# Kernel optimization log

Hardware: AMD Instinct MI355X
Metric: run time of the kernel (lower is better)

## Reference

```python
import jax, jax.numpy as jnp
import numpy as np

NUM_HEADS = 8

def _ln(x):
    m = x.mean(-1, keepdims=True)
    v = ((x - m) ** 2).mean(-1, keepdims=True)
    return (x - m) / jnp.sqrt(v + 1e-5)

def _encoder_layer(x, qkv_w, out_w, w1, w2, attn_mask=None):
    # standard post-LN transformer encoder layer; returns output and
    # head-averaged attention probabilities (b, t, t)
    b, t, d = x.shape
    dh = d // NUM_HEADS
    qkv = jnp.einsum('btd,cde->cbte', x, qkv_w)          # (3, b, t, d)
    q, k, v = [a.reshape(b, t, NUM_HEADS, dh).transpose(0, 2, 1, 3) for a in qkv]
    scores = jnp.einsum('bhqd,bhkd->bhqk', q, k) / jnp.sqrt(jnp.asarray(dh, x.dtype))
    if attn_mask is not None:
        scores = scores + attn_mask                       # additive -inf/0 mask
    probs = jax.nn.softmax(scores, axis=-1)
    ctx = jnp.einsum('bhqk,bhkd->bhqd', probs, v)
    ctx = ctx.transpose(0, 2, 1, 3).reshape(b, t, d)
    x = _ln(x + ctx @ out_w)
    x = _ln(x + jax.nn.relu(x @ w1) @ w2)
    return x, probs.mean(axis=1)

def _window_ids(wbool):
    # faithful vectorization of generate_local_window_mask_v2's sequential scan:
    # run-length segmentation of the thresholded weights, where a run of
    # length 1 is absorbed into the following run (weights[frame_start] is
    # overwritten). Returns per-frame window id (T,) int32.
    T = wbool.shape[0]
    def step(carry, t):
        cur, start, wid = carry
        wt = wbool[t]
        same = wt == cur
        merge = (~same) & (start + 1 == t)   # length-1 run absorbed
        close = (~same) & (~merge)           # close window, start new one
        cur = jnp.where(same, cur, wt)
        start = jnp.where(close, t, start)
        wid = wid + close.astype(jnp.int32)
        return (cur, start, wid), wid
    _, ids = jax.lax.scan(step, (wbool[0], jnp.int32(0), jnp.int32(0)), jnp.arange(1, T))
    return jnp.concatenate([jnp.zeros((1,), jnp.int32), ids])

def reference(x, v_qkv_w, v_out_w, v_w1, v_w2, l_qkv_w, l_out_w, l_w1, l_w2):
    b, t, d = x.shape
    # 1) vanilla transformer pass
    out_v, aw_v = _encoder_layer(x, v_qkv_w, v_out_w, v_w1, v_w2)
    # attention received per key token, min-max normalized (normalize_tensor)
    w = aw_v.sum(axis=1)                                   # (b, t)
    wmin = w.min(axis=-1, keepdims=True)
    wmax = w.max(axis=-1, keepdims=True)
    w = (w - wmin) / (wmax - wmin + 1e-8)
    # 2) dynamic window mask generation (threshold = 0.5)
    ids = jax.vmap(_window_ids)(w >= 0.5)                  # (b, t)
    same = ids[:, :, None] == ids[:, None, :]
    attn_mask = jnp.where(same, 0.0, -jnp.inf).astype(x.dtype)   # (b, t, t)
    # window_mapping[b, k, j] = 1 if frame j belongs to window k
    # (kept at full t rows; torch truncates to max_window_count, which is
    #  data-dependent; extra rows here are all-zero)
    window_mapping = (jnp.arange(t, dtype=jnp.int32)[None, :, None] == ids[:, None, :]).astype(x.dtype)
    # 3) dynamic-local-window transformer pass with block-diagonal mask
    out_l, aw_l = _encoder_layer(out_v, l_qkv_w, l_out_w, l_w1, l_w2,
                                 attn_mask=attn_mask[:, None])  # broadcast over heads
    aw_l = jnp.where(jnp.isneginf(aw_l), jnp.zeros_like(aw_l), aw_l)
    wl = jax.nn.softmax(aw_l.sum(axis=1), axis=-1)         # (b, t)
    # 4) window-weighted pooling
    word_tokens = jnp.einsum('bwt,btd->bwd', window_mapping, out_l * wl[:, :, None])
    return jnp.concatenate([word_tokens, x], axis=1), window_mapping

def setup_inputs() -> dict:
    B, T, D, FF = 8, 1024, 512, 2048
    key = jax.random.key(0)
    ks = jax.random.split(key, 9)
    s = 0.02
    return {
        'x': jax.random.normal(ks[0], (B, T, D), jnp.float32),
        'v_qkv_w': jax.random.normal(ks[1], (3, D, D), jnp.float32) * s,
        'v_out_w': jax.random.normal(ks[2], (D, D), jnp.float32) * s,
        'v_w1': jax.random.normal(ks[3], (D, FF), jnp.float32) * s,
        'v_w2': jax.random.normal(ks[4], (FF, D), jnp.float32) * s,
        'l_qkv_w': jax.random.normal(ks[5], (3, D, D), jnp.float32) * s,
        'l_out_w': jax.random.normal(ks[6], (D, D), jnp.float32) * s,
        'l_w1': jax.random.normal(ks[7], (D, FF), jnp.float32) * s,
        'l_w2': jax.random.normal(ks[8], (FF, D), jnp.float32) * s,
    }
```

## Files before the change

kernel.cpp:

```cpp
#include <hip/hip_runtime.h>
#include <math.h>

#define Bz 8
#define Tz 1024
#define Dz 512
#define FFz 2048
#define Hz 8
#define DHz 64
#define Mz (Bz * Tz)

typedef __attribute__((ext_vector_type(8))) short short8;
typedef __attribute__((ext_vector_type(4))) float f32x4;

__device__ inline unsigned short f2bf(float f) {
  unsigned u = __builtin_bit_cast(unsigned, f);
  return (unsigned short)((u + 0x7FFFu + ((u >> 16) & 1u)) >> 16);
}
__device__ inline float bf2f(unsigned short h) {
  unsigned u = (unsigned)h << 16;
  return __builtin_bit_cast(float, u);
}

__device__ inline void gll16(const unsigned short* g, unsigned short* l) {
  __builtin_amdgcn_global_load_lds(
      (const __attribute__((address_space(1))) void*)g,
      (__attribute__((address_space(3))) void*)l, 16, 0, 0);
}

__device__ inline void attn_decode(int g, int& b, int& h, int& qt) {
  const int xcd = g & 7;
  const int j = g >> 3;
  qt = j & 15;
  const int bh = ((j >> 4) << 3) | xcd;
  b = bh >> 3;
  h = bh & 7;
}

__device__ inline int swz(int row, int slotByte) {
  return row * 128 + (slotByte ^ ((row & 7) << 4));
}

struct WDesc { const float* src; unsigned short* dst; unsigned short* dstlo;
               int K; int N; int blk0; };
struct PrepArgs { WDesc d[12]; int nwc; };

__global__ __launch_bounds__(256) void prep_kernel(PrepArgs P,
    const float* __restrict__ x, unsigned short* __restrict__ xbf,
    unsigned short* __restrict__ xlo, float* __restrict__ csz)
{
  const int bid = blockIdx.x;
  const int tid = threadIdx.x;
  if (bid < P.nwc) {
    int i = 0;
    while (i < 11 && bid >= P.d[i + 1].blk0) ++i;
    const WDesc w = P.d[i];
    const int lb = bid - w.blk0;
    const int nbn = w.N / 32;
    const int bn = (lb % nbn) * 32, bk = (lb / nbn) * 32;
    __shared__ float t[32][33];
    const int tx = tid & 31, ty = tid >> 5;
#pragma unroll
    for (int r = 0; r < 32; r += 8)
      t[ty + r][tx] = w.src[(size_t)(bk + ty + r) * w.N + bn + tx];
    __syncthreads();
#pragma unroll
    for (int r = 0; r < 32; r += 8) {
      float v = t[tx][ty + r];
      unsigned short hv = f2bf(v);
      w.dst[(size_t)(bn + ty + r) * w.K + bk + tx] = hv;
      if (w.dstlo)
        w.dstlo[(size_t)(bn + ty + r) * w.K + bk + tx] = f2bf(v - bf2f(hv));
    }
  } else if (bid < P.nwc + 64) {
    int idx = (bid - P.nwc) * 256 + tid;
    csz[idx] = 0.f;
  } else {
    int i = (bid - P.nwc - 64) * 256 + tid;
    float4 v = *reinterpret_cast<const float4*>(&x[(size_t)i * 4]);
    ushort4 o, ol;
    o.x = f2bf(v.x); o.y = f2bf(v.y); o.z = f2bf(v.z); o.w = f2bf(v.w);
    ol.x = f2bf(v.x - bf2f(o.x)); ol.y = f2bf(v.y - bf2f(o.y));
    ol.z = f2bf(v.z - bf2f(o.z)); ol.w = f2bf(v.w - bf2f(o.w));
    *reinterpret_cast<ushort4*>(&xbf[(size_t)i * 4]) = o;
    *reinterpret_cast<ushort4*>(&xlo[(size_t)i * 4]) = ol;
  }
}

__global__ __launch_bounds__(256) void mfma_gemm_kernel(
    const unsigned short* __restrict__ A, const unsigned short* __restrict__ BT,
    void* __restrict__ p1, void* __restrict__ p2, void* __restrict__ p3,
    int K, int N, int mode)
{
  __shared__ unsigned short As[128 * 32];
  __shared__ unsigned short Bs[128 * 32];
  const int tid = threadIdx.x;
  const int lane = tid & 63, wave = tid >> 6;
  const int mr = lane & 15, quad = lane >> 4;
  const int wr = wave >> 1, wc = wave & 1;
  const int m0 = blockIdx.y * 128;
  const int n0 = blockIdx.x * 128;

  f32x4 acc[4][4];
  const f32x4 zero = {0.f, 0.f, 0.f, 0.f};
#pragma unroll
  for (int i = 0; i < 4; ++i)
#pragma unroll
    for (int j = 0; j < 4; ++j) acc[i][j] = zero;

  const int lrow = lane >> 2, lslot = lane & 3;
  const unsigned short* Ag0 = A + (size_t)(m0 + wave * 16 + lrow) * K + lslot * 8;
  const unsigned short* Ag1 = A + (size_t)(m0 + 64 + wave * 16 + lrow) * K + lslot * 8;
  const unsigned short* Bg0 = BT + (size_t)(n0 + wave * 16 + lrow) * K + lslot * 8;
  const unsigned short* Bg1 = BT + (size_t)(n0 + 64 + wave * 16 + lrow) * K + lslot * 8;
  unsigned short* Al0 = As + wave * 512;
  unsigned short* Al1 = As + 2048 + wave * 512;
  unsigned short* Bl0 = Bs + wave * 512;
  unsigned short* Bl1 = Bs + 2048 + wave * 512;
  char* AsB = (char*)As;
  char* BsB = (char*)Bs;

  for (int k0 = 0; k0 < K; k0 += 32) {
    gll16(Ag0 + k0, Al0);
    gll16(Ag1 + k0, Al1);
    gll16(Bg0 + k0, Bl0);
    gll16(Bg1 + k0, Bl1);
    __syncthreads();
    short8 af[4], bf[4];
#pragma unroll
    for (int i = 0; i < 4; ++i)
      af[i] = *reinterpret_cast<const short8*>(AsB + (wr * 64 + i * 16 + mr) * 64 + quad * 16);
#pragma unroll
    for (int j = 0; j < 4; ++j)
      bf[j] = *reinterpret_cast<const short8*>(BsB + (wc * 64 + j * 16 + mr) * 64 + quad * 16);
#pragma unroll
    for (int i = 0; i < 4; ++i)
#pragma unroll
      for (int j = 0; j < 4; ++j)
        acc[i][j] = __builtin_amdgcn_mfma_f32_16x16x32_bf16(af[i], bf[j], acc[i][j], 0, 0, 0);
    __syncthreads();
  }

  const int m0w = m0 + wr * 64;
  const int n0w = n0 + wc * 64;
  int emode = mode;
  unsigned short* Cbf = (unsigned short*)p1;
  unsigned short* Vt  = (unsigned short*)p1;
  int ncol = N, coff = 0;
  if (mode == 5) {
    if (n0w < 512)       { emode = 1; Cbf = (unsigned short*)p1; ncol = 512; coff = 0; }
    else if (n0w < 1024) { emode = 1; Cbf = (unsigned short*)p2; ncol = 512; coff = 512; }
    else                 { emode = 4; Vt = (unsigned short*)p3; coff = 1024; }
  }
  if (emode == 4) {
#pragma unroll
    for (int i = 0; i < 4; ++i)
#pragma unroll
      for (int j = 0; j < 4; ++j) {
        const int col = n0w - coff + j * 16 + mr;
        const int row0 = m0w + i * 16 + quad * 4;
        const int bb = row0 >> 10, t0 = row0 & 1023;
        ushort4 pk;
        pk.x = f2bf(acc[i][j][0]); pk.y = f2bf(acc[i][j][1]);
        pk.z = f2bf(acc[i][j][2]); pk.w = f2bf(acc[i][j][3]);
        *reinterpret_cast<ushort4*>(
            &Vt[((size_t)((bb * Hz + (col >> 6)) * DHz + (col & 63))) * Tz + t0]) = pk;
      }
  } else if (emode == 0) {
    float* Cf = (float*)p1;
#pragma unroll
    for (int i = 0; i < 4; ++i)
#pragma unroll
      for (int j = 0; j < 4; ++j) {
        const int col = n0w + j * 16 + mr;
#pragma unroll
        for (int rr = 0; rr < 4; ++rr)
          Cf[(size_t)(m0w + i * 16 + quad * 4 + rr) * N + col] = acc[i][j][rr];
      }
  } else {
    const bool relu = (emode == 2);
#pragma unroll
    for (int i = 0; i < 4; ++i)
#pragma unroll
      for (int j = 0; j < 4; ++j) {
        const int col = n0w - coff + j * 16 + mr;
#pragma unroll
        for (int rr = 0; rr < 4; ++rr) {
          float v = acc[i][j][rr];
          if (relu) v = fmaxf(v, 0.f);
          Cbf[(size_t)(m0w + i * 16 + quad * 4 + rr) * ncol + col] = f2bf(v);
        }
      }
  }
}

__global__ __launch_bounds__(256) void gemm_qk_mfma_kernel(
    const unsigned short* __restrict__ Xh, const unsigned short* __restrict__ Xl,
    const unsigned short* __restrict__ WQh, const unsigned short* __restrict__ WQl,
    const unsigned short* __restrict__ WKh, const unsigned short* __restrict__ WKl,
    unsigned short* __restrict__ Qhi, unsigned short* __restrict__ Qlo,
    unsigned short* __restrict__ Khi, unsigned short* __restrict__ Klo)
{
  __shared__ unsigned short Ash[128 * 32];
  __shared__ unsigned short Asl[128 * 32];
  __shared__ unsigned short Bsh[128 * 32];
  __shared__ unsigned short Bsl[128 * 32];
  const int tid = threadIdx.x;
  const int lane = tid & 63, wave = tid >> 6;
  const int mr = lane & 15, quad = lane >> 4;
  const int wr = wave >> 1, wc = wave & 1;
  const int sel = blockIdx.y >> 6;
  const int m0 = (blockIdx.y & 63) * 128;
  const int n0 = blockIdx.x * 128;
  const unsigned short* Bh = sel ? WKh : WQh;
  const unsigned short* Bl = sel ? WKl : WQl;
  unsigned short* Chi = sel ? Khi : Qhi;
  unsigned short* Clo = sel ? Klo : Qlo;

  f32x4 acc[4][4];
  const f32x4 zero = {0.f, 0.f, 0.f, 0.f};
#pragma unroll
  for (int i = 0; i < 4; ++i)
#pragma unroll
    for (int j = 0; j < 4; ++j) acc[i][j] = zero;

  const int lrow = lane >> 2, lslot = lane & 3;
  const unsigned short* gAh0 = Xh + (size_t)(m0 + wave * 16 + lrow) * Dz + lslot * 8;
  const unsigned short* gAh1 = Xh + (size_t)(m0 + 64 + wave * 16 + lrow) * Dz + lslot * 8;
  const unsigned short* gAl0 = Xl + (size_t)(m0 + wave * 16 + lrow) * Dz + lslot * 8;
  const unsigned short* gAl1 = Xl + (size_t)(m0 + 64 + wave * 16 + lrow) * Dz + lslot * 8;
  const unsigned short* gBh0 = Bh + (size_t)(n0 + wave * 16 + lrow) * Dz + lslot * 8;
  const unsigned short* gBh1 = Bh + (size_t)(n0 + 64 + wave * 16 + lrow) * Dz + lslot * 8;
  const unsigned short* gBl0 = Bl + (size_t)(n0 + wave * 16 + lrow) * Dz + lslot * 8;
  const unsigned short* gBl1 = Bl + (size_t)(n0 + 64 + wave * 16 + lrow) * Dz + lslot * 8;
  unsigned short* LAh0 = Ash + wave * 512; unsigned short* LAh1 = Ash + 2048 + wave * 512;
  unsigned short* LAl0 = Asl + wave * 512; unsigned short* LAl1 = Asl + 2048 + wave * 512;
  unsigned short* LBh0 = Bsh + wave * 512; unsigned short* LBh1 = Bsh + 2048 + wave * 512;
  unsigned short* LBl0 = Bsl + wave * 512; unsigned short* LBl1 = Bsl + 2048 + wave * 512;
  char* AhB = (char*)Ash; char* AlB = (char*)Asl;
  char* BhB = (char*)Bsh; char* BlB = (char*)Bsl;

  for (int k0 = 0; k0 < Dz; k0 += 32) {
    gll16(gAh0 + k0, LAh0); gll16(gAh1 + k0, LAh1);
    gll16(gAl0 + k0, LAl0); gll16(gAl1 + k0, LAl1);
    gll16(gBh0 + k0, LBh0); gll16(gBh1 + k0, LBh1);
    gll16(gBl0 + k0, LBl0); gll16(gBl1 + k0, LBl1);
    __syncthreads();
    short8 ah[4], al[4], bh[4], bl[4];
#pragma unroll
    for (int i = 0; i < 4; ++i) {
      const int ab = (wr * 64 + i * 16 + mr) * 64 + quad * 16;
      ah[i] = *reinterpret_cast<const short8*>(AhB + ab);
      al[i] = *reinterpret_cast<const short8*>(AlB + ab);
    }
#pragma unroll
    for (int j = 0; j < 4; ++j) {
      const int bb = (wc * 64 + j * 16 + mr) * 64 + quad * 16;
      bh[j] = *reinterpret_cast<const short8*>(BhB + bb);
      bl[j] = *reinterpret_cast<const short8*>(BlB + bb);
    }
#pragma unroll
    for (int i = 0; i < 4; ++i)
#pragma unroll
      for (int j = 0; j < 4; ++j) {
        acc[i][j] = __builtin_amdgcn_mfma_f32_16x16x32_bf16(al[i], bh[j], acc[i][j], 0, 0, 0);
        acc[i][j] = __builtin_amdgcn_mfma_f32_16x16x32_bf16(ah[i], bl[j], acc[i][j], 0, 0, 0);
        acc[i][j] = __builtin_amdgcn_mfma_f32_16x16x32_bf16(ah[i], bh[j], acc[i][j], 0, 0, 0);
      }
    __syncthreads();
  }

  const int m0w = m0 + wr * 64;
  const int n0w = n0 + wc * 64;
#pragma unroll
  for (int i = 0; i < 4; ++i)
#pragma unroll
    for (int j = 0; j < 4; ++j) {
      const int col = n0w + j * 16 + mr;
#pragma unroll
      for (int rr = 0; rr < 4; ++rr) {
        const size_t row = (size_t)(m0w + i * 16 + quad * 4 + rr);
        float v = acc[i][j][rr];
        unsigned short hv = f2bf(v);
        Chi[row * Dz + col] = hv;
        Clo[row * Dz + col] = f2bf(v - bf2f(hv));
      }
    }
}

__global__ __launch_bounds__(256) void attn_z_kernel(
    const unsigned short* __restrict__ Qh, const unsigned short* __restrict__ Kh,
    float* __restrict__ invzG)
{
  __shared__ unsigned short Ksh[64 * 64];
  const int tid = threadIdx.x;
  const int lane = tid & 63, wave = tid >> 6;
  const int c = lane & 15, quad = lane >> 4;
  int b, h, qt;
  attn_decode(blockIdx.x, b, h, qt);
  const size_t bT = (size_t)b * Tz;
  const int qrow = qt * 64 + wave * 16;
  const int hoff = h * DHz;

  const size_t qbase = (bT + qrow + c) * Dz + hoff + quad * 8;
  short8 q0 = *reinterpret_cast<const short8*>(Qh + qbase);
  short8 q1 = *reinterpret_cast<const short8*>(Qh + qbase + 32);

  const int sr = tid >> 3;
  const int sj = (tid & 7) * 16;
  const unsigned short* khb = Kh + (bT + sr) * Dz + hoff + (tid & 7) * 8;
  char* KshB = (char*)Ksh;

  const f32x4 zf = {0.f, 0.f, 0.f, 0.f};
  float z[4] = {0.f, 0.f, 0.f, 0.f};

  for (int t = 0; t < 16; ++t) {
    const int k0 = t * 64;
    short8 g0 = *reinterpret_cast<const short8*>(khb + (size_t)k0 * Dz);
    short8 g1 = *reinterpret_cast<const short8*>(khb + (size_t)(k0 + 32) * Dz);
    *reinterpret_cast<short8*>(KshB + swz(sr, sj)) = g0;
    *reinterpret_cast<short8*>(KshB + swz(sr + 32, sj)) = g1;
    __syncthreads();
#pragma unroll
    for (int sub = 0; sub < 4; ++sub) {
      const int row = sub * 16 + c;
      short8 kh0 = *reinterpret_cast<const short8*>(KshB + swz(row, quad * 16));
      short8 kh1 = *reinterpret_cast<const short8*>(KshB + swz(row, 64 + quad * 16));
      f32x4 aA = zf, aB = zf;
      aA = __builtin_amdgcn_mfma_f32_16x16x32_bf16(q0, kh0, aA, 0, 0, 0);
      aB = __builtin_amdgcn_mfma_f32_16x16x32_bf16(q1, kh1, aB, 0, 0, 0);
#pragma unroll
      for (int rr = 0; rr < 4; ++rr) z[rr] += __expf((aA[rr] + aB[rr]) * 0.125f);
    }
    __syncthreads();
  }
#pragma unroll
  for (int w = 1; w < 16; w <<= 1) {
#pragma unroll
    for (int rr = 0; rr < 4; ++rr) z[rr] += __shfl_xor(z[rr], w);
  }
  if (c == 0) {
#pragma unroll
    for (int rr = 0; rr < 4; ++rr)
      invzG[(size_t)(b * Hz + h) * Tz + qrow + quad * 4 + rr] = 1.f / z[rr];
  }
}

__global__ __launch_bounds__(256) void attn_ctx_kernel(
    const unsigned short* __restrict__ Qh, const unsigned short* __restrict__ Ql,
    const unsigned short* __restrict__ Kh, const unsigned short* __restrict__ Kl,
    const unsigned short* __restrict__ Vt, const float* __restrict__ invzG,
    unsigned short* __restrict__ ctx, float* __restrict__ part)
{
  __shared__ unsigned short Ksh[64 * 64];
  __shared__ unsigned short Ksl[64 * 64];
  __shared__ unsigned short Vsh[64 * 64];
  __shared__ unsigned short Pld[64][76];
  __shared__ float CSPt[4][64];
  const int tid = threadIdx.x;
  const int lane = tid & 63, wave = tid >> 6;
  const int c = lane & 15, quad = lane >> 4;
  int b, h, qt;
  attn_decode(blockIdx.x, b, h, qt);
  const size_t bT = (size_t)b * Tz;
  const int qrow = qt * 64 + wave * 16;
  const int hoff = h * DHz;
  const int lidx = b * 128 + h * 16 + qt;

  const size_t qbase = (bT + qrow + c) * Dz + hoff + quad * 8;
  short8 q0h = *reinterpret_cast<const short8*>(Qh + qbase);
  short8 q1h = *reinterpret_cast<const short8*>(Qh + qbase + 32);
  short8 q0l = *reinterpret_cast<const short8*>(Ql + qbase);
  short8 q1l = *reinterpret_cast<const short8*>(Ql + qbase + 32);

  float invz[4];
#pragma unroll
  for (int rr = 0; rr < 4; ++rr)
    invz[rr] = invzG[(size_t)(b * Hz + h) * Tz + qrow + quad * 4 + rr];

  const int sr = tid >> 3;
  const int sj = (tid & 7) * 16;
  const unsigned short* khb = Kh + (bT + sr) * Dz + hoff + (tid & 7) * 8;
  const unsigned short* klb = Kl + (bT + sr) * Dz + hoff + (tid & 7) * 8;
  const unsigned short* vtb = Vt + ((size_t)(b * Hz + h) * DHz + sr) * Tz + (tid & 7) * 8;

  const f32x4 zf = {0.f, 0.f, 0.f, 0.f};
  f32x4 ot[4] = {zf, zf, zf, zf};

  char* KshB = (char*)Ksh;
  char* KslB = (char*)Ksl;
  char* VshB = (char*)Vsh;

  for (int t = 0; t < 16; ++t) {
    const int k0 = t * 64;
    short8 g0 = *reinterpret_cast<const short8*>(khb + (size_t)k0 * Dz);
    short8 g1 = *reinterpret_cast<const short8*>(khb + (size_t)(k0 + 32) * Dz);
    short8 g2 = *reinterpret_cast<const short8*>(klb + (size_t)k0 * Dz);
    short8 g3 = *reinterpret_cast<const short8*>(klb + (size_t)(k0 + 32) * Dz);
    short8 g4 = *reinterpret_cast<const short8*>(vtb + k0);
    short8 g5 = *reinterpret_cast<const short8*>(vtb + 32 * Tz + k0);
    *reinterpret_cast<short8*>(KshB + swz(sr, sj)) = g0;
    *reinterpret_cast<short8*>(KshB + swz(sr + 32, sj)) = g1;
    *reinterpret_cast<short8*>(KslB + swz(sr, sj)) = g2;
    *reinterpret_cast<short8*>(KslB + swz(sr + 32, sj)) = g3;
    *reinterpret_cast<short8*>(VshB + swz(sr, sj)) = g4;
    *reinterpret_cast<short8*>(VshB + swz(sr + 32, sj)) = g5;
    __syncthreads();

#pragma unroll
    for (int sub = 0; sub < 4; ++sub) {
      const int row = sub * 16 + c;
      short8 kh0 = *reinterpret_cast<const short8*>(KshB + swz(row, quad * 16));
      short8 kh1 = *reinterpret_cast<const short8*>(KshB + swz(row, 64 + quad * 16));
      short8 kl0 = *reinterpret_cast<const short8*>(KslB + swz(row, quad * 16));
      short8 kl1 = *reinterpret_cast<const short8*>(KslB + swz(row, 64 + quad * 16));
      f32x4 aA = zf, aB = zf;
      aA = __builtin_amdgcn_mfma_f32_16x16x32_bf16(q0h, kh0, aA, 0, 0, 0);
      aB = __builtin_amdgcn_mfma_f32_16x16x32_bf16(q1h, kh1, aB, 0, 0, 0);
      aA = __builtin_amdgcn_mfma_f32_16x16x32_bf16(q0h, kl0, aA, 0, 0, 0);
      aB = __builtin_amdgcn_mfma_f32_16x16x32_bf16(q1h, kl1, aB, 0, 0, 0);
      aA = __builtin_amdgcn_mfma_f32_16x16x32_bf16(q0l, kh0, aA, 0, 0, 0);
      aB = __builtin_amdgcn_mfma_f32_16x16x32_bf16(q1l, kh1, aB, 0, 0, 0);
      float p[4];
#pragma unroll
      for (int rr = 0; rr < 4; ++rr)
        p[rr] = __expf((aA[rr] + aB[rr]) * 0.125f) * invz[rr];
      float cs = p[0] + p[1] + p[2] + p[3];
      cs += __shfl_xor(cs, 16);
      cs += __shfl_xor(cs, 32);
      if (quad == 0) CSPt[wave][sub * 16 + c] = cs;
#pragma unroll
      for (int rr = 0; rr < 4; ++rr)
        Pld[(wave << 4) + quad * 4 + rr][sub * 16 + c] = f2bf(p[rr]);
    }

    union { short8 v; ushort4 hh[2]; } pb0, pb1;
    pb0.hh[0] = *reinterpret_cast<const ushort4*>(&Pld[(wave << 4) + c][quad * 8]);
    pb0.hh[1] = *reinterpret_cast<const ushort4*>(&Pld[(wave << 4) + c][quad * 8 + 4]);
    pb1.hh[0] = *reinterpret_cast<const ushort4*>(&Pld[(wave << 4) + c][32 + quad * 8]);
    pb1.hh[1] = *reinterpret_cast<const ushort4*>(&Pld[(wave << 4) + c][32 + quad * 8 + 4]);
#pragma unroll
    for (int ds = 0; ds < 4; ++ds) {
      const int row = ds * 16 + c;
      short8 v0 = *reinterpret_cast<const short8*>(VshB + swz(row, quad * 16));
      short8 v1 = *reinterpret_cast<const short8*>(VshB + swz(row, 64 + quad * 16));
      ot[ds] = __builtin_amdgcn_mfma_f32_16x16x32_bf16(v0, pb0.v, ot[ds], 0, 0, 0);
      ot[ds] = __builtin_amdgcn_mfma_f32_16x16x32_bf16(v1, pb1.v, ot[ds], 0, 0, 0);
    }
    __syncthreads();

    if (tid < 64) {
      float v = ((CSPt[0][tid] + CSPt[1][tid]) + CSPt[2][tid]) + CSPt[3][tid];
      part[(size_t)lidx * 1024 + k0 + tid] = v * (1.f / Hz);
    }
  }

  const size_t cb = (bT + qrow + c) * Dz + hoff;
#pragma unroll
  for (int ds = 0; ds < 4; ++ds) {
    ushort4 pk;
    pk.x = f2bf(ot[ds][0]); pk.y = f2bf(ot[ds][1]);
    pk.z = f2bf(ot[ds][2]); pk.w = f2bf(ot[ds][3]);
    *reinterpret_cast<ushort4*>(&ctx[cb + ds * 16 + quad * 4]) = pk;
  }
}

__global__ __launch_bounds__(256) void colsum_reduce_kernel(
    const float* __restrict__ part, float* __restrict__ colsum)
{
  const int i = blockIdx.x * 256 + threadIdx.x;
  const int b = i >> 10, k = i & 1023;
  const float* p = part + (size_t)(b * 128) * 1024 + k;
  float s = 0.f;
  for (int j = 0; j < 128; ++j) s += p[(size_t)j * 1024];
  colsum[i] = s;
}

__global__ __launch_bounds__(256) void attn_mfma2_kernel(
    const unsigned short* __restrict__ Qh, const unsigned short* __restrict__ Kh,
    const unsigned short* __restrict__ Vt, const int* __restrict__ ids,
    const int* __restrict__ wst,
    unsigned short* __restrict__ ctx, float* __restrict__ colsum)
{
  __shared__ unsigned short Ksh[64 * 64];
  __shared__ unsigned short Vsh[64 * 64];
  __shared__ unsigned short Pld[64][76];
  __shared__ float csb[1024];

  const int tid = threadIdx.x;
  const int lane = tid & 63, wave = tid >> 6;
  const int c = lane & 15, quad = lane >> 4;
  int b, h, qt;
  attn_decode(blockIdx.x, b, h, qt);
  const size_t bT = (size_t)b * Tz;
  const int qrow = qt * 64 + wave * 16;
  const int hoff = h * DHz;

  for (int i = tid; i < 1024; i += 256) csb[i] = 0.f;

  const int id_lo = ids[bT + qt * 64];
  const int id_hi = ids[bT + qt * 64 + 63];
  const int klo = wst[b * (Tz + 1) + id_lo];
  const int khi = wst[b * (Tz + 1) + id_hi + 1];
  const int t0 = klo >> 6, t1 = (khi - 1) >> 6;

  const size_t qbase = (bT + qrow + c) * Dz + hoff + quad * 8;
  short8 q0 = *reinterpret_cast<const short8*>(Qh + qbase);
  short8 q1 = *reinterpret_cast<const short8*>(Qh + qbase + 32);

  int qid[4];
#pragma unroll
  for (int rr = 0; rr < 4; ++rr) qid[rr] = ids[bT + qrow + quad * 4 + rr];

  const int sr = tid >> 3;
  const int sj = (tid & 7) * 16;
  const unsigned short* khb = Kh + (bT + sr) * Dz + hoff + (tid & 7) * 8;
  const unsigned short* vtb = Vt + ((size_t)(b * Hz + h) * DHz + sr) * Tz + (tid & 7) * 8;
  char* KshB = (char*)Ksh;
  char* VshB = (char*)Vsh;
  __syncthreads();

  const f32x4 zf = {0.f, 0.f, 0.f, 0.f};

  float z[4] = {0.f, 0.f, 0.f, 0.f};
  for (int t = t0; t <= t1; ++t) {
    const int k0 = t * 64;
    short8 g0 = *reinterpret_cast<const short8*>(khb + (size_t)k0 * Dz);
    short8 g1 = *reinterpret_cast<const short8*>(khb + (size_t)(k0 + 32) * Dz);
    *reinterpret_cast<short8*>(KshB + swz(sr, sj)) = g0;
    *reinterpret_cast<short8*>(KshB + swz(sr + 32, sj)) = g1;
    __syncthreads();
#pragma unroll
    for (int sub = 0; sub < 4; ++sub) {
      const int row = sub * 16 + c;
      short8 kh0 = *reinterpret_cast<const short8*>(KshB + swz(row, quad * 16));
      short8 kh1 = *reinterpret_cast<const short8*>(KshB + swz(row, 64 + quad * 16));
      f32x4 acc = zf;
      acc = __builtin_amdgcn_mfma_f32_16x16x32_bf16(q0, kh0, acc, 0, 0, 0);
      acc = __builtin_amdgcn_mfma_f32_16x16x32_bf16(q1, kh1, acc, 0, 0, 0);
      int kidv = ids[bT + k0 + sub * 16 + c];
#pragma unroll
      for (int rr = 0; rr < 4; ++rr) {
        float e = __expf(acc[rr] * 0.125f);
        if (qid[rr] != kidv) e = 0.f;
        z[rr] += e;
      }
    }
    __syncthreads();
  }
#pragma unroll
  for (int w = 1; w < 16; w <<= 1) {
#pragma unroll
    for (int rr = 0; rr < 4; ++rr) z[rr] += __shfl_xor(z[rr], w);
  }
  float invz[4];
#pragma unroll
  for (int rr = 0; rr < 4; ++rr) invz[rr] = 1.f / z[rr];

  f32x4 ot[4] = {zf, zf, zf, zf};
  for (int t = t0; t <= t1; ++t) {
    const int k0 = t * 64;
    short8 g0 = *reinterpret_cast<const short8*>(khb + (size_t)k0 * Dz);
    short8 g1 = *reinterpret_cast<const short8*>(khb + (size_t)(k0 + 32) * Dz);
    short8 g4 = *reinterpret_cast<const short8*>(vtb + k0);
    short8 g5 = *reinterpret_cast<const short8*>(vtb + 32 * Tz + k0);
    *reinterpret_cast<short8*>(KshB + swz(sr, sj)) = g0;
    *reinterpret_cast<short8*>(KshB + swz(sr + 32, sj)) = g1;
    *reinterpret_cast<short8*>(VshB + swz(sr, sj)) = g4;
    *reinterpret_cast<short8*>(VshB + swz(sr + 32, sj)) = g5;
    __syncthreads();
#pragma unroll
    for (int sub = 0; sub < 4; ++sub) {
      const int row = sub * 16 + c;
      short8 kh0 = *reinterpret_cast<const short8*>(KshB + swz(row, quad * 16));
      short8 kh1 = *reinterpret_cast<const short8*>(KshB + swz(row, 64 + quad * 16));
      f32x4 acc = zf;
      acc = __builtin_amdgcn_mfma_f32_16x16x32_bf16(q0, kh0, acc, 0, 0, 0);
      acc = __builtin_amdgcn_mfma_f32_16x16x32_bf16(q1, kh1, acc, 0, 0, 0);
      int kidv = ids[bT + k0 + sub * 16 + c];
      float p[4];
#pragma unroll
      for (int rr = 0; rr < 4; ++rr) {
        float e = __expf(acc[rr] * 0.125f);
        if (qid[rr] != kidv) e = 0.f;
        p[rr] = e * invz[rr];
      }
      float cs = p[0] + p[1] + p[2] + p[3];
      cs += __shfl_xor(cs, 16);
      cs += __shfl_xor(cs, 32);
      if (quad == 0) atomicAdd(&csb[k0 + sub * 16 + c], cs);
#pragma unroll
      for (int rr = 0; rr < 4; ++rr)
        Pld[(wave << 4) + quad * 4 + rr][sub * 16 + c] = f2bf(p[rr]);
    }
    union { short8 v; ushort4 hh[2]; } pb0, pb1;
    pb0.hh[0] = *reinterpret_cast<const ushort4*>(&Pld[(wave << 4) + c][quad * 8]);
    pb0.hh[1] = *reinterpret_cast<const ushort4*>(&Pld[(wave << 4) + c][quad * 8 + 4]);
    pb1.hh[0] = *reinterpret_cast<const ushort4*>(&Pld[(wave << 4) + c][32 + quad * 8]);
    pb1.hh[1] = *reinterpret_cast<const ushort4*>(&Pld[(wave << 4) + c][32 + quad * 8 + 4]);
#pragma unroll
    for (int ds = 0; ds < 4; ++ds) {
      const int row = ds * 16 + c;
      short8 v0 = *reinterpret_cast<const short8*>(VshB + swz(row, quad * 16));
      short8 v1 = *reinterpret_cast<const short8*>(VshB + swz(row, 64 + quad * 16));
      ot[ds] = __builtin_amdgcn_mfma_f32_16x16x32_bf16(v0, pb0.v, ot[ds], 0, 0, 0);
      ot[ds] = __builtin_amdgcn_mfma_f32_16x16x32_bf16(v1, pb1.v, ot[ds], 0, 0, 0);
    }
    __syncthreads();
  }

  const size_t cb = (bT + qrow + c) * Dz + hoff;
#pragma unroll
  for (int ds = 0; ds < 4; ++ds) {
    ushort4 pk;
    pk.x = f2bf(ot[ds][0]); pk.y = f2bf(ot[ds][1]);
    pk.z = f2bf(ot[ds][2]); pk.w = f2bf(ot[ds][3]);
    *reinterpret_cast<ushort4*>(&ctx[cb + ds * 16 + quad * 4]) = pk;
  }
  __syncthreads();
  for (int i = tid; i < 1024; i += 256)
    atomicAdd(&colsum[bT + i], csb[i] * (1.f / Hz));
}

__global__ __launch_bounds__(256) void ln_kernel(const float* __restrict__ residf,
    const unsigned short* __restrict__ residbf, const float* __restrict__ delta,
    float* __restrict__ outf, unsigned short* __restrict__ outbf)
{
  const size_t base = (size_t)blockIdx.x * Dz;
  const int tid = threadIdx.x;
  float r0, r1;
  if (residf) {
    r0 = residf[base + tid]; r1 = residf[base + tid + 256];
  } else {
    r0 = bf2f(residbf[base + tid]); r1 = bf2f(residbf[base + tid + 256]);
  }
  float x0 = r0 + delta[base + tid];
  float x1 = r1 + delta[base + tid + 256];
  __shared__ float red[4];
  float s = x0 + x1;
#pragma unroll
  for (int off = 32; off; off >>= 1) s += __shfl_down(s, off);
  if ((tid & 63) == 0) red[tid >> 6] = s;
  __syncthreads();
  const float mean = (red[0] + red[1] + red[2] + red[3]) * (1.f / Dz);
  __syncthreads();
  float d0 = x0 - mean, d1 = x1 - mean;
  float v = d0 * d0 + d1 * d1;
#pragma unroll
  for (int off = 32; off; off >>= 1) v += __shfl_down(v, off);
  if ((tid & 63) == 0) red[tid >> 6] = v;
  __syncthreads();
  const float var = (red[0] + red[1] + red[2] + red[3]) * (1.f / Dz);
// ... 118 lines not shown
    const int b = bid >> 10;
    float a0 = 0.f, a1 = 0.f;
    if (w < nwin[b]) {
      const int s = wst[b * (Tz + 1) + w], e = wst[b * (Tz + 1) + w + 1];
      for (int t = s; t < e; ++t) {
        const float sc = wl[b * Tz + t];
        const unsigned short* p = &outl[((size_t)(b * Tz + t)) * Dz];
        a0 += bf2f(p[tid]) * sc;
        a1 += bf2f(p[tid + 256]) * sc;
      }
    }
    float* o = &out[((size_t)(b * 2 * Tz + w)) * Dz];
    o[tid] = a0;
    o[tid + 256] = a1;
  } else if (bid < 16384) {
    const int lb = bid - 8192;
    const int w = lb & (Tz - 1);
    const int b = lb >> 10;
    const int j = tid * 4;
    int4 id4 = *reinterpret_cast<const int4*>(&ids[b * Tz + j]);
    float4 v;
    v.x = (id4.x == w) ? 1.f : 0.f;
    v.y = (id4.y == w) ? 1.f : 0.f;
    v.z = (id4.z == w) ? 1.f : 0.f;
    v.w = (id4.w == w) ? 1.f : 0.f;
    *reinterpret_cast<float4*>(&out2[((size_t)(b * Tz + w)) * Tz + j]) = v;
  } else {
    size_t i = (size_t)(bid - 16384) * 256 + tid;
    size_t idx = i * 4;
    size_t rowi = idx >> 9;
    size_t d = idx & 511;
    size_t b = rowi >> 10, t = rowi & 1023;
    float4 v = *reinterpret_cast<const float4*>(&x[idx]);
    *reinterpret_cast<float4*>(&out[(((b * 2 * Tz) + Tz + t) << 9) + d]) = v;
  }
}

extern "C" void kernel_launch(void* const* d_in, const int* in_sizes, int n_in,
                              void* d_out, int out_size, void* d_ws, size_t ws_size,
                              hipStream_t stream)
{
  (void)in_sizes; (void)n_in; (void)out_size; (void)ws_size;
  const float* x     = (const float*)d_in[0];
  const float* vqkv  = (const float*)d_in[1];
  const float* voutw = (const float*)d_in[2];
  const float* vw1   = (const float*)d_in[3];
  const float* vw2   = (const float*)d_in[4];
  const float* lqkv  = (const float*)d_in[5];
  const float* loutw = (const float*)d_in[6];
  const float* lw1   = (const float*)d_in[7];
  const float* lw2   = (const float*)d_in[8];
  float* out = (float*)d_out;
  float* ws  = (float*)d_ws;

  unsigned short* QLbf = (unsigned short*)(ws + 0);
  unsigned short* KLbf = (unsigned short*)(ws + 2097152);
  float* PROJ = ws + 0;
  float* Y1   = ws + 4194304;
  unsigned short* QHbf = (unsigned short*)(ws + 8388608);
  unsigned short* KHbf = (unsigned short*)(ws + 10485760);
  unsigned short* VT   = (unsigned short*)(ws + 12582912);
  unsigned short* SLOT1 = (unsigned short*)(ws + 14680064);
  unsigned short* SLOT2 = (unsigned short*)(ws + 16777216);
  unsigned short* HIDbf = (unsigned short*)(ws + 18874368);
  unsigned short* XBF   = (unsigned short*)(ws + 18874368);
  float* PART = ws + 18874368;
  unsigned short* XLO = (unsigned short*)(ws + 20971520);
  unsigned short* WVQV = (unsigned short*)(ws + 27262976);
  unsigned short* WVO  = (unsigned short*)(ws + 27394048);
  unsigned short* WV1  = (unsigned short*)(ws + 27525120);
  unsigned short* WV2  = (unsigned short*)(ws + 28049408);
  unsigned short* WLQ0 = (unsigned short*)(ws + 28573696);
  unsigned short* WLQ1 = (unsigned short*)(ws + 28704768);
  unsigned short* WLQ2 = (unsigned short*)(ws + 28835840);
  unsigned short* WLO  = (unsigned short*)(ws + 28966912);
  unsigned short* WL1  = (unsigned short*)(ws + 29097984);
  unsigned short* WL2  = (unsigned short*)(ws + 29622272);
  float* CS1   = ws + 30146560;
  float* CS2   = ws + 30154752;
  float* WLs   = ws + 30162944;
  int*   IDS   = (int*)(ws + 30171136);
  int*   WST   = (int*)(ws + 30179328);
  int*   NWIN  = (int*)(ws + 30187776);
  float* INVZ  = ws + 30195968;
  unsigned short* WQH = (unsigned short*)(ws + 30261504);
  unsigned short* WQL = (unsigned short*)(ws + 30392576);
  unsigned short* WKH = (unsigned short*)(ws + 30523648);
  unsigned short* WKL = (unsigned short*)(ws + 30654720);

  dim3 blk(256);

  PrepArgs P;
  auto setw = [&](int i, const float* s, unsigned short* d, unsigned short* dl,
                  int K, int N, int b0) {
    P.d[i].src = s; P.d[i].dst = d; P.d[i].dstlo = dl;
    P.d[i].K = K; P.d[i].N = N; P.d[i].blk0 = b0;
  };
  int b0 = 0;
  setw(0, vqkv + 2 * Dz * Dz, WVQV, nullptr, Dz, Dz, b0); b0 += 256;
  setw(1, voutw, WVO, nullptr, Dz, Dz, b0); b0 += 256;
  setw(2, vw1, WV1, nullptr, Dz, FFz, b0); b0 += 1024;
  setw(3, vw2, WV2, nullptr, FFz, Dz, b0); b0 += 1024;
  setw(4, lqkv + 0 * Dz * Dz, WLQ0, nullptr, Dz, Dz, b0); b0 += 256;
  setw(5, lqkv + 1 * Dz * Dz, WLQ1, nullptr, Dz, Dz, b0); b0 += 256;
  setw(6, lqkv + 2 * Dz * Dz, WLQ2, nullptr, Dz, Dz, b0); b0 += 256;
  setw(7, loutw, WLO, nullptr, Dz, Dz, b0); b0 += 256;
  setw(8, lw1, WL1, nullptr, Dz, FFz, b0); b0 += 1024;
  setw(9, lw2, WL2, nullptr, FFz, Dz, b0); b0 += 1024;
  setw(10, vqkv + 0 * Dz * Dz, WQH, WQL, Dz, Dz, b0); b0 += 256;
  setw(11, vqkv + 1 * Dz * Dz, WKH, WKL, Dz, Dz, b0); b0 += 256;
  P.nwc = b0;
  prep_kernel<<<dim3(P.nwc + 64 + 4096), blk, 0, stream>>>(P, x, XBF, XLO, CS1);

  auto mgemm = [&](const unsigned short* A, const unsigned short* BT, void* p1,
                   void* p2, void* p3, int K, int N, int mode) {
    mfma_gemm_kernel<<<dim3(N / 128, Mz / 128), dim3(256), 0, stream>>>(
        A, BT, p1, p2, p3, K, N, mode);
  };

  gemm_qk_mfma_kernel<<<dim3(4, 128), dim3(256), 0, stream>>>(
      XBF, XLO, WQH, WQL, WKH, WKL, QHbf, QLbf, KHbf, KLbf);
  attn_z_kernel<<<dim3(Bz * Hz * 16), blk, 0, stream>>>(QHbf, KHbf, INVZ);
  mgemm(XBF, WVQV, VT, nullptr, nullptr, Dz, Dz, 4);
  attn_ctx_kernel<<<dim3(Bz * Hz * 16), blk, 0, stream>>>(
      QHbf, QLbf, KHbf, KLbf, VT, INVZ, SLOT1, PART);
  colsum_reduce_kernel<<<dim3(32), blk, 0, stream>>>(PART, CS1);
  window_ids_kernel<<<dim3(Bz), blk, 0, stream>>>(CS1, IDS, WST, NWIN);
  mgemm(SLOT1, WVO, PROJ, nullptr, nullptr, Dz, Dz, 0);
  ln_kernel<<<dim3(Mz), blk, 0, stream>>>(x, nullptr, PROJ, Y1, SLOT2);
  mgemm(SLOT2, WV1, HIDbf, nullptr, nullptr, Dz, FFz, 2);
  mgemm(HIDbf, WV2, PROJ, nullptr, nullptr, FFz, Dz, 0);
  ln_kernel<<<dim3(Mz), blk, 0, stream>>>(Y1, nullptr, PROJ, nullptr, SLOT2);

  mgemm(SLOT2, WLQ0, QHbf, KHbf, VT, Dz, 3 * Dz, 5);
  attn_mfma2_kernel<<<dim3(Bz * Hz * 16), blk, 0, stream>>>(
      QHbf, KHbf, VT, IDS, WST, SLOT1, CS2);
  mgemm(SLOT1, WLO, PROJ, nullptr, nullptr, Dz, Dz, 0);
  ln_kernel<<<dim3(Mz), blk, 0, stream>>>(nullptr, SLOT2, PROJ, Y1, SLOT2);
  mgemm(SLOT2, WL1, HIDbf, nullptr, nullptr, Dz, FFz, 2);
  mgemm(HIDbf, WL2, PROJ, nullptr, nullptr, FFz, Dz, 0);
  ln_kernel<<<dim3(Mz), blk, 0, stream>>>(Y1, nullptr, PROJ, nullptr, SLOT2);

  wl_softmax_kernel<<<dim3(Bz), blk, 0, stream>>>(CS2, WLs);
  outputs_kernel<<<dim3(20480), blk, 0, stream>>>(SLOT2, WLs, WST, NWIN, IDS, x,
                                                  out, out + (size_t)Bz * 2 * Tz * Dz);
}
```

Measured before the change: 582.5 us.

## Widen GEMM K-tile to 64 with swizzled LDS, fuse attention normalizer pass, use async LDS loads

The GEMM kernels now stage a 64-wide K slice per iteration into an XOR-swizzled LDS layout, which halves the number of barriers and should reduce bank conflicts. LDS use per block doubles. The separate attention normalizer kernel is folded into the context kernel as a first pass, removing one launch and the INVZ round-trip through memory. The attention kernels also switch from register-staged global loads to direct global-to-LDS loads with a matching swizzle.

```diff
diff --git a/kernel.cpp b/kernel.cpp
--- a/kernel.cpp
+++ b/kernel.cpp
@@ -91,8 +91,8 @@
     void* __restrict__ p1, void* __restrict__ p2, void* __restrict__ p3,
     int K, int N, int mode)
 {
-  __shared__ unsigned short As[128 * 32];
-  __shared__ unsigned short Bs[128 * 32];
+  __shared__ unsigned short As[128 * 64];
+  __shared__ unsigned short Bs[128 * 64];
   const int tid = threadIdx.x;
   const int lane = tid & 63, wave = tid >> 6;
   const int mr = lane & 15, quad = lane >> 4;
@@ -107,36 +107,42 @@
 #pragma unroll
     for (int j = 0; j < 4; ++j) acc[i][j] = zero;
 
-  const int lrow = lane >> 2, lslot = lane & 3;
-  const unsigned short* Ag0 = A + (size_t)(m0 + wave * 16 + lrow) * K + lslot * 8;
-  const unsigned short* Ag1 = A + (size_t)(m0 + 64 + wave * 16 + lrow) * K + lslot * 8;
-  const unsigned short* Bg0 = BT + (size_t)(n0 + wave * 16 + lrow) * K + lslot * 8;
-  const unsigned short* Bg1 = BT + (size_t)(n0 + 64 + wave * 16 + lrow) * K + lslot * 8;
-  unsigned short* Al0 = As + wave * 512;
-  unsigned short* Al1 = As + 2048 + wave * 512;
-  unsigned short* Bl0 = Bs + wave * 512;
-  unsigned short* Bl1 = Bs + 2048 + wave * 512;
+  const int r8 = lane >> 3;
+  const int s8 = (lane & 7) ^ r8;
+  const unsigned short* Agb = A + (size_t)(m0 + wave * 8 + r8) * K + s8 * 8;
+  const unsigned short* Bgb = BT + (size_t)(n0 + wave * 8 + r8) * K + s8 * 8;
+  unsigned short* Adb = As + wave * 512;
+  unsigned short* Bdb = Bs + wave * 512;
   char* AsB = (char*)As;
   char* BsB = (char*)Bs;
-
-  for (int k0 = 0; k0 < K; k0 += 32) {
-    gll16(Ag0 + k0, Al0);
-    gll16(Ag1 + k0, Al1);
-    gll16(Bg0 + k0, Bl0);
-    gll16(Bg1 + k0, Bl1);
-    __syncthreads();
-    short8 af[4], bf[4];
-#pragma unroll
-    for (int i = 0; i < 4; ++i)
-      af[i] = *reinterpret_cast<const short8*>(AsB + (wr * 64 + i * 16 + mr) * 64 + quad * 16);
-#pragma unroll
-    for (int j = 0; j < 4; ++j)
-      bf[j] = *reinterpret_cast<const short8*>(BsB + (wc * 64 + j * 16 + mr) * 64 + quad * 16);
-#pragma unroll
-    for (int i = 0; i < 4; ++i)
+  const int xr = (mr & 7) << 4;
+
+  for (int k0 = 0; k0 < K; k0 += 64) {
+#pragma unroll
+    for (int p = 0; p < 4; ++p) {
+      gll16(Agb + (size_t)(p * 32) * K + k0, Adb + p * 2048);
+      gll16(Bgb + (size_t)(p * 32) * K + k0, Bdb + p * 2048);
+    }
+    __syncthreads();
+    short8 af[2][4], bf[2][4];
+#pragma unroll
+    for (int hh = 0; hh < 2; ++hh) {
+#pragma unroll
+      for (int i = 0; i < 4; ++i)
+        af[hh][i] = *reinterpret_cast<const short8*>(
+            AsB + (wr * 64 + i * 16 + mr) * 128 + ((((hh << 2) + quad) << 4) ^ xr));
 #pragma unroll
       for (int j = 0; j < 4; ++j)
-        acc[i][j] = __builtin_amdgcn_mfma_f32_16x16x32_bf16(af[i], bf[j], acc[i][j], 0, 0, 0);
+        bf[hh][j] = *reinterpret_cast<const short8*>(
+            BsB + (wc * 64 + j * 16 + mr) * 128 + ((((hh << 2) + quad) << 4) ^ xr));
+    }
+#pragma unroll
+    for (int hh = 0; hh < 2; ++hh)
+#pragma unroll
+      for (int i = 0; i < 4; ++i)
+#pragma unroll
+        for (int j = 0; j < 4; ++j)
+          acc[i][j] = __builtin_amdgcn_mfma_f32_16x16x32_bf16(af[hh][i], bf[hh][j], acc[i][j], 0, 0, 0);
     __syncthreads();
   }
 
@@ -200,10 +206,10 @@
     unsigned short* __restrict__ Qhi, unsigned short* __restrict__ Qlo,
     unsigned short* __restrict__ Khi, unsigned short* __restrict__ Klo)
 {
-  __shared__ unsigned short Ash[128 * 32];
-  __shared__ unsigned short Asl[128 * 32];
-  __shared__ unsigned short Bsh[128 * 32];
-  __shared__ unsigned short Bsl[128 * 32];
+  __shared__ unsigned short Ash[128 * 64];
+  __shared__ unsigned short Asl[128 * 64];
+  __shared__ unsigned short Bsh[128 * 64];
+  __shared__ unsigned short Bsl[128 * 64];
   const int tid = threadIdx.x;
   const int lane = tid & 63, wave = tid >> 6;
   const int mr = lane & 15, quad = lane >> 4;
@@ -223,49 +229,55 @@
 #pragma unroll
     for (int j = 0; j < 4; ++j) acc[i][j] = zero;
 
-  const int lrow = lane >> 2, lslot = lane & 3;
-  const unsigned short* gAh0 = Xh + (size_t)(m0 + wave * 16 + lrow) * Dz + lslot * 8;
-  const unsigned short* gAh1 = Xh + (size_t)(m0 + 64 + wave * 16 + lrow) * Dz + lslot * 8;
-  const unsigned short* gAl0 = Xl + (size_t)(m0 + wave * 16 + lrow) * Dz + lslot * 8;
-  const unsigned short* gAl1 = Xl + (size_t)(m0 + 64 + wave * 16 + lrow) * Dz + lslot * 8;
-  const unsigned short* gBh0 = Bh + (size_t)(n0 + wave * 16 + lrow) * Dz + lslot * 8;
-  const unsigned short* gBh1 = Bh + (size_t)(n0 + 64 + wave * 16 + lrow) * Dz + lslot * 8;
-  const unsigned short* gBl0 = Bl + (size_t)(n0 + wave * 16 + lrow) * Dz + lslot * 8;
-  const unsigned short* gBl1 = Bl + (size_t)(n0 + 64 + wave * 16 + lrow) * Dz + lslot * 8;
-  unsigned short* LAh0 = Ash + wave * 512; unsigned short* LAh1 = Ash + 2048 + wave * 512;
-  unsigned short* LAl0 = Asl + wave * 512; unsigned short* LAl1 = Asl + 2048 + wave * 512;
-  unsigned short* LBh0 = Bsh + wave * 512; unsigned short* LBh1 = Bsh + 2048 + wave * 512;
-  unsigned short* LBl0 = Bsl + wave * 512; unsigned short* LBl1 = Bsl + 2048 + wave * 512;
+  const int r8 = lane >> 3;
+  const int s8 = (lane & 7) ^ r8;
+  const unsigned short* gAh = Xh + (size_t)(m0 + wave * 8 + r8) * Dz + s8 * 8;
+  const unsigned short* gAl = Xl + (size_t)(m0 + wave * 8 + r8) * Dz + s8 * 8;
+  const unsigned short* gBh = Bh + (size_t)(n0 + wave * 8 + r8) * Dz + s8 * 8;
+  const unsigned short* gBl = Bl + (size_t)(n0 + wave * 8 + r8) * Dz + s8 * 8;
+  unsigned short* dAh = Ash + wave * 512;
+  unsigned short* dAl = Asl + wave * 512;
+  unsigned short* dBh = Bsh + wave * 512;
+  unsigned short* dBl = Bsl + wave * 512;
   char* AhB = (char*)Ash; char* AlB = (char*)Asl;
   char* BhB = (char*)Bsh; char* BlB = (char*)Bsl;
-
-  for (int k0 = 0; k0 < Dz; k0 += 32) {
-    gll16(gAh0 + k0, LAh0); gll16(gAh1 + k0, LAh1);
-    gll16(gAl0 + k0, LAl0); gll16(gAl1 + k0, LAl1);
-    gll16(gBh0 + k0, LBh0); gll16(gBh1 + k0, LBh1);
-    gll16(gBl0 + k0, LBl0); gll16(gBl1 + k0, LBl1);
-    __syncthreads();
-    short8 ah[4], al[4], bh[4], bl[4];
-#pragma unroll
-    for (int i = 0; i < 4; ++i) {
-      const int ab = (wr * 64 + i * 16 + mr) * 64 + quad * 16;
-      ah[i] = *reinterpret_cast<const short8*>(AhB + ab);
-      al[i] = *reinterpret_cast<const short8*>(AlB + ab);
-    }
-#pragma unroll
-    for (int j = 0; j < 4; ++j) {
-      const int bb = (wc * 64 + j * 16 + mr) * 64 + quad * 16;
-      bh[j] = *reinterpret_cast<const short8*>(BhB + bb);
-      bl[j] = *reinterpret_cast<const short8*>(BlB + bb);
-    }
-#pragma unroll
-    for (int i = 0; i < 4; ++i)
+  const int xr = (mr & 7) << 4;
+
+  for (int k0 = 0; k0 < Dz; k0 += 64) {
+#pragma unroll
+    for (int p = 0; p < 4; ++p) {
+      gll16(gAh + (size_t)(p * 32) * Dz + k0, dAh + p * 2048);
+      gll16(gAl + (size_t)(p * 32) * Dz + k0, dAl + p * 2048);
+      gll16(gBh + (size_t)(p * 32) * Dz + k0, dBh + p * 2048);
+      gll16(gBl + (size_t)(p * 32) * Dz + k0, dBl + p * 2048);
+    }
+    __syncthreads();
+    short8 ah[2][4], al[2][4], bh[2][4], bl[2][4];
+#pragma unroll
+    for (int hh = 0; hh < 2; ++hh) {
+#pragma unroll
+      for (int i = 0; i < 4; ++i) {
+        const int ab = (wr * 64 + i * 16 + mr) * 128 + ((((hh << 2) + quad) << 4) ^ xr);
+        ah[hh][i] = *reinterpret_cast<const short8*>(AhB + ab);
+        al[hh][i] = *reinterpret_cast<const short8*>(AlB + ab);
+      }
 #pragma unroll
       for (int j = 0; j < 4; ++j) {
-        acc[i][j] = __builtin_amdgcn_mfma_f32_16x16x32_bf16(al[i], bh[j], acc[i][j], 0, 0, 0);
-        acc[i][j] = __builtin_amdgcn_mfma_f32_16x16x32_bf16(ah[i], bl[j], acc[i][j], 0, 0, 0);
-        acc[i][j] = __builtin_amdgcn_mfma_f32_16x16x32_bf16(ah[i], bh[j], acc[i][j], 0, 0, 0);
-      }
+        const int bb = (wc * 64 + j * 16 + mr) * 128 + ((((hh << 2) + quad) << 4) ^ xr);
+        bh[hh][j] = *reinterpret_cast<const short8*>(BhB + bb);
+        bl[hh][j] = *reinterpret_cast<const short8*>(BlB + bb);
+      }
+    }
+#pragma unroll
+    for (int hh = 0; hh < 2; ++hh)
+#pragma unroll
+      for (int i = 0; i < 4; ++i)
+#pragma unroll
+        for (int j = 0; j < 4; ++j) {
+          acc[i][j] = __builtin_amdgcn_mfma_f32_16x16x32_bf16(al[hh][i], bh[hh][j], acc[i][j], 0, 0, 0);
+          acc[i][j] = __builtin_amdgcn_mfma_f32_16x16x32_bf16(ah[hh][i], bl[hh][j], acc[i][j], 0, 0, 0);
+          acc[i][j] = __builtin_amdgcn_mfma_f32_16x16x32_bf16(ah[hh][i], bh[hh][j], acc[i][j], 0, 0, 0);
+        }
     __syncthreads();
   }
 
@@ -287,68 +299,10 @@
     }
 }
 
-__global__ __launch_bounds__(256) void attn_z_kernel(
-    const unsigned short* __restrict__ Qh, const unsigned short* __restrict__ Kh,
-    float* __restrict__ invzG)
-{
-  __shared__ unsigned short Ksh[64 * 64];
-  const int tid = threadIdx.x;
-  const int lane = tid & 63, wave = tid >> 6;
-  const int c = lane & 15, quad = lane >> 4;
-  int b, h, qt;
-  attn_decode(blockIdx.x, b, h, qt);
-  const size_t bT = (size_t)b * Tz;
-  const int qrow = qt * 64 + wave * 16;
-  const int hoff = h * DHz;
-
-  const size_t qbase = (bT + qrow + c) * Dz + hoff + quad * 8;
-  short8 q0 = *reinterpret_cast<const short8*>(Qh + qbase);
-  short8 q1 = *reinterpret_cast<const short8*>(Qh + qbase + 32);
-
-  const int sr = tid >> 3;
-  const int sj = (tid & 7) * 16;
-  const unsigned short* khb = Kh + (bT + sr) * Dz + hoff + (tid & 7) * 8;
-  char* KshB = (char*)Ksh;
-
-  const f32x4 zf = {0.f, 0.f, 0.f, 0.f};
-  float z[4] = {0.f, 0.f, 0.f, 0.f};
-
-  for (int t = 0; t < 16; ++t) {
-    const int k0 = t * 64;
-    short8 g0 = *reinterpret_cast<const short8*>(khb + (size_t)k0 * Dz);
-    short8 g1 = *reinterpret_cast<const short8*>(khb + (size_t)(k0 + 32) * Dz);
-    *reinterpret_cast<short8*>(KshB + swz(sr, sj)) = g0;
-    *reinterpret_cast<short8*>(KshB + swz(sr + 32, sj)) = g1;
-    __syncthreads();
-#pragma unroll
-    for (int sub = 0; sub < 4; ++sub) {
-      const int row = sub * 16 + c;
-      short8 kh0 = *reinterpret_cast<const short8*>(KshB + swz(row, quad * 16));
-      short8 kh1 = *reinterpret_cast<const short8*>(KshB + swz(row, 64 + quad * 16));
-      f32x4 aA = zf, aB = zf;
-      aA = __builtin_amdgcn_mfma_f32_16x16x32_bf16(q0, kh0, aA, 0, 0, 0);
-      aB = __builtin_amdgcn_mfma_f32_16x16x32_bf16(q1, kh1, aB, 0, 0, 0);
-#pragma unroll
-      for (int rr = 0; rr < 4; ++rr) z[rr] += __expf((aA[rr] + aB[rr]) * 0.125f);
-    }
-    __syncthreads();
-  }
-#pragma unroll
-  for (int w = 1; w < 16; w <<= 1) {
-#pragma unroll
-    for (int rr = 0; rr < 4; ++rr) z[rr] += __shfl_xor(z[rr], w);
-  }
-  if (c == 0) {
-#pragma unroll
-    for (int rr = 0; rr < 4; ++rr)
-      invzG[(size_t)(b * Hz + h) * Tz + qrow + quad * 4 + rr] = 1.f / z[rr];
-  }
-}
-
-__global__ __launch_bounds__(256) void attn_ctx_kernel(
+__global__ __launch_bounds__(256) void attn_fused_kernel(
     const unsigned short* __restrict__ Qh, const unsigned short* __restrict__ Ql,
     const unsigned short* __restrict__ Kh, const unsigned short* __restrict__ Kl,
-    const unsigned short* __restrict__ Vt, const float* __restrict__ invzG,
+    const unsigned short* __restrict__ Vt,
     unsigned short* __restrict__ ctx, float* __restrict__ part)
 {
   __shared__ unsigned short Ksh[64 * 64];
@@ -372,38 +326,57 @@
   short8 q0l = *reinterpret_cast<const short8*>(Ql + qbase);
   short8 q1l = *reinterpret_cast<const short8*>(Ql + qbase + 32);
 
-  float invz[4];
-#pragma unroll
-  for (int rr = 0; rr < 4; ++rr)
-    invz[rr] = invzG[(size_t)(b * Hz + h) * Tz + qrow + quad * 4 + rr];
-
-  const int sr = tid >> 3;
-  const int sj = (tid & 7) * 16;
-  const unsigned short* khb = Kh + (bT + sr) * Dz + hoff + (tid & 7) * 8;
-  const unsigned short* klb = Kl + (bT + sr) * Dz + hoff + (tid & 7) * 8;
-  const unsigned short* vtb = Vt + ((size_t)(b * Hz + h) * DHz + sr) * Tz + (tid & 7) * 8;
-
-  const f32x4 zf = {0.f, 0.f, 0.f, 0.f};
-  f32x4 ot[4] = {zf, zf, zf, zf};
-
+  const int r8 = lane >> 3;
+  const int s8 = (lane & 7) ^ r8;
+  const unsigned short* khg = Kh + (bT + wave * 8 + r8) * Dz + hoff + s8 * 8;
+  const unsigned short* klg = Kl + (bT + wave * 8 + r8) * Dz + hoff + s8 * 8;
+  const unsigned short* vtg = Vt + ((size_t)((b * Hz + h) * DHz) + wave * 8 + r8) * Tz + s8 * 8;
+  unsigned short* KshW = Ksh + wave * 512;
+  unsigned short* KslW = Ksl + wave * 512;
+  unsigned short* VshW = Vsh + wave * 512;
   char* KshB = (char*)Ksh;
   char* KslB = (char*)Ksl;
   char* VshB = (char*)Vsh;
 
+  const f32x4 zf = {0.f, 0.f, 0.f, 0.f};
+
+  float z[4] = {0.f, 0.f, 0.f, 0.f};
   for (int t = 0; t < 16; ++t) {
     const int k0 = t * 64;
-    short8 g0 = *reinterpret_cast<const short8*>(khb + (size_t)k0 * Dz);
-    short8 g1 = *reinterpret_cast<const short8*>(khb + (size_t)(k0 + 32) * Dz);
-    short8 g2 = *reinterpret_cast<const short8*>(klb + (size_t)k0 * Dz);
-    short8 g3 = *reinterpret_cast<const short8*>(klb + (size_t)(k0 + 32) * Dz);
-    short8 g4 = *reinterpret_cast<const short8*>(vtb + k0);
-    short8 g5 = *reinterpret_cast<const short8*>(vtb + 32 * Tz + k0);
-    *reinterpret_cast<short8*>(KshB + swz(sr, sj)) = g0;
-    *reinterpret_cast<short8*>(KshB + swz(sr + 32, sj)) = g1;
-    *reinterpret_cast<short8*>(KslB + swz(sr, sj)) = g2;
-    *reinterpret_cast<short8*>(KslB + swz(sr + 32, sj)) = g3;
-    *reinterpret_cast<short8*>(VshB + swz(sr, sj)) = g4;
-    *reinterpret_cast<short8*>(VshB + swz(sr + 32, sj)) = g5;
+    gll16(khg + (size_t)k0 * Dz, KshW);
+    gll16(khg + (size_t)(k0 + 32) * Dz, KshW + 2048);
+    __syncthreads();
+#pragma unroll
+    for (int sub = 0; sub < 4; ++sub) {
+      const int row = sub * 16 + c;
+      short8 kh0 = *reinterpret_cast<const short8*>(KshB + swz(row, quad * 16));
+      short8 kh1 = *reinterpret_cast<const short8*>(KshB + swz(row, 64 + quad * 16));
+      f32x4 aA = zf, aB = zf;
+      aA = __builtin_amdgcn_mfma_f32_16x16x32_bf16(q0h, kh0, aA, 0, 0, 0);
+      aB = __builtin_amdgcn_mfma_f32_16x16x32_bf16(q1h, kh1, aB, 0, 0, 0);
+#pragma unroll
+      for (int rr = 0; rr < 4; ++rr) z[rr] += __expf((aA[rr] + aB[rr]) * 0.125f);
+    }
+    __syncthreads();
+  }
+#pragma unroll
+  for (int w = 1; w < 16; w <<= 1) {
+#pragma unroll
+    for (int rr = 0; rr < 4; ++rr) z[rr] += __shfl_xor(z[rr], w);
+  }
+  float invz[4];
+#pragma unroll
+  for (int rr = 0; rr < 4; ++rr) invz[rr] = 1.f / z[rr];
+
+  f32x4 ot[4] = {zf, zf, zf, zf};
+  for (int t = 0; t < 16; ++t) {
+    const int k0 = t * 64;
+    gll16(khg + (size_t)k0 * Dz, KshW);
+    gll16(khg + (size_t)(k0 + 32) * Dz, KshW + 2048);
+    gll16(klg + (size_t)k0 * Dz, KslW);
+    gll16(klg + (size_t)(k0 + 32) * Dz, KslW + 2048);
+    gll16(vtg + k0, VshW);
+    gll16(vtg + (size_t)32 * Tz + k0, VshW + 2048);
     __syncthreads();
 
 #pragma unroll
@@ -511,10 +484,12 @@
 #pragma unroll
   for (int rr = 0; rr < 4; ++rr) qid[rr] = ids[bT + qrow + quad * 4 + rr];
 
-  const int sr = tid >> 3;
-  const int sj = (tid & 7) * 16;
-  const unsigned short* khb = Kh + (bT + sr) * Dz + hoff + (tid & 7) * 8;
-  const unsigned short* vtb = Vt + ((size_t)(b * Hz + h) * DHz + sr) * Tz + (tid & 7) * 8;
+  const int r8 = lane >> 3;
+  const int s8 = (lane & 7) ^ r8;
+  const unsigned short* khg = Kh + (bT + wave * 8 + r8) * Dz + hoff + s8 * 8;
+  const unsigned short* vtg = Vt + ((size_t)((b * Hz + h) * DHz) + wave * 8 + r8) * Tz + s8 * 8;
+  unsigned short* KshW = Ksh + wave * 512;
+  unsigned short* VshW = Vsh + wave * 512;
   char* KshB = (char*)Ksh;
   char* VshB = (char*)Vsh;
   __syncthreads();
@@ -524,10 +499,8 @@
   float z[4] = {0.f, 0.f, 0.f, 0.f};
   for (int t = t0; t <= t1; ++t) {
     const int k0 = t * 64;
-    short8 g0 = *reinterpret_cast<const short8*>(khb + (size_t)k0 * Dz);
-    short8 g1 = *reinterpret_cast<const short8*>(khb + (size_t)(k0 + 32) * Dz);
-    *reinterpret_cast<short8*>(KshB + swz(sr, sj)) = g0;
-    *reinterpret_cast<short8*>(KshB + swz(sr + 32, sj)) = g1;
+    gll16(khg + (size_t)k0 * Dz, KshW);
+    gll16(khg + (size_t)(k0 + 32) * Dz, KshW + 2048);
     __syncthreads();
 #pragma unroll
     for (int sub = 0; sub < 4; ++sub) {
@@ -559,14 +532,10 @@
   f32x4 ot[4] = {zf, zf, zf, zf};
   for (int t = t0; t <= t1; ++t) {
     const int k0 = t * 64;
-    short8 g0 = *reinterpret_cast<const short8*>(khb + (size_t)k0 * Dz);
-    short8 g1 = *reinterpret_cast<const short8*>(khb + (size_t)(k0 + 32) * Dz);
-    short8 g4 = *reinterpret_cast<const short8*>(vtb + k0);
-    short8 g5 = *reinterpret_cast<const short8*>(vtb + 32 * Tz + k0);
-    *reinterpret_cast<short8*>(KshB + swz(sr, sj)) = g0;
-    *reinterpret_cast<short8*>(KshB + swz(sr + 32, sj)) = g1;
-    *reinterpret_cast<short8*>(VshB + swz(sr, sj)) = g4;
-    *reinterpret_cast<short8*>(VshB + swz(sr + 32, sj)) = g5;
+    gll16(khg + (size_t)k0 * Dz, KshW);
+    gll16(khg + (size_t)(k0 + 32) * Dz, KshW + 2048);
+    gll16(vtg + k0, VshW);
+    gll16(vtg + (size_t)32 * Tz + k0, VshW + 2048);
     __syncthreads();
 #pragma unroll
     for (int sub = 0; sub < 4; ++sub) {
@@ -851,7 +820,6 @@
   int*   IDS   = (int*)(ws + 30171136);
   int*   WST   = (int*)(ws + 30179328);
   int*   NWIN  = (int*)(ws + 30187776);
-  float* INVZ  = ws + 30195968;
   unsigned short* WQH = (unsigned short*)(ws + 30261504);
   unsigned short* WQL = (unsigned short*)(ws + 30392576);
   unsigned short* WKH = (unsigned short*)(ws + 30523648);
@@ -889,10 +857,9 @@
 
   gemm_qk_mfma_kernel<<<dim3(4, 128), dim3(256), 0, stream>>>(
       XBF, XLO, WQH, WQL, WKH, WKL, QHbf, QLbf, KHbf, KLbf);
-  attn_z_kernel<<<dim3(Bz * Hz * 16), blk, 0, stream>>>(QHbf, KHbf, INVZ);
   mgemm(XBF, WVQV, VT, nullptr, nullptr, Dz, Dz, 4);
-  attn_ctx_kernel<<<dim3(Bz * Hz * 16), blk, 0, stream>>>(
-      QHbf, QLbf, KHbf, KLbf, VT, INVZ, SLOT1, PART);
+  attn_fused_kernel<<<dim3(Bz * Hz * 16), blk, 0, stream>>>(
+      QHbf, QLbf, KHbf, KLbf, VT, SLOT1, PART);
   colsum_reduce_kernel<<<dim3(32), blk, 0, stream>>>(PART, CS1);
   window_ids_kernel<<<dim3(Bz), blk, 0, stream>>>(CS1, IDS, WST, NWIN);
   mgemm(SLOT1, WVO, PROJ, nullptr, nullptr, Dz, Dz, 0);
```

Result: faster. 540.1 us (-7.3%).
